# Kernel optimization log

Measured on AMD Instinct MI355X. Metric: run time of the kernel, lower is better.

Reference implementation:

```python
import jax, jax.numpy as jnp
import numpy as np

NEG_INF = -1e30
EPS = 1e-7  # keras.backend.epsilon()

B, T, C, L = 256, 1024, 128, 128


def setup_inputs() -> dict:
    key = jax.random.key(0)
    k1, k2, k3, k4 = jax.random.split(key, 4)
    # ctc_batch_cost expects softmax probabilities in y_pred
    y_pred = jax.nn.softmax(jax.random.normal(k1, (B, T, C), dtype=jnp.float32), axis=-1)
    y_true = jax.random.randint(k2, (B, L), 0, C - 1)           # blank = C-1 excluded from labels
    input_length = jax.random.randint(k3, (B, 1), T // 2, T + 1)
    label_length = jax.random.randint(k4, (B, 1), L // 2, L + 1)
    return {"y_true": y_true, "y_pred": y_pred,
            "input_length": input_length, "label_length": label_length}


def _ctc_batch_cost(y_true, y_pred, input_length, label_length):
    """Faithful jax version of keras.backend.ctc_batch_cost (blank = num_classes-1)."""
    b, t_max, c = y_pred.shape
    l_max = y_true.shape[1]
    s_max = 2 * l_max + 1
    blank = c - 1

    logp = jnp.log(y_pred + EPS)                                # [B,T,C]

    # Extended label sequence: blank, l0, blank, l1, ..., blank  -> [B,S]
    ext = jnp.full((b, s_max), blank, dtype=y_true.dtype)
    ext = ext.at[:, 1::2].set(y_true)

    # Gather log-probs of extended labels per time step -> [B,T,S]
    lp_ext = jnp.take_along_axis(logp, ext[:, None, :], axis=2)

    # Skip transition (s-2 -> s) allowed iff ext[s] != blank and ext[s] != ext[s-2]
    same = jnp.concatenate([jnp.ones((b, 2), bool), ext[:, 2:] == ext[:, :-2]], axis=1)
    skip_ok = (ext != blank) & (~same)                          # [B,S]

    # Valid extended positions given per-sample label_length
    s_idx = jnp.arange(s_max)
    valid_s = s_idx[None, :] < (2 * label_length + 1)           # [B,S]

    ll = label_length[:, 0]
    il = input_length[:, 0]

    alpha0 = jnp.full((b, s_max), NEG_INF, dtype=logp.dtype)
    alpha0 = alpha0.at[:, 0].set(lp_ext[:, 0, 0])
    alpha0 = alpha0.at[:, 1].set(jnp.where(ll > 0, lp_ext[:, 0, 1], NEG_INF))

    neg1 = jnp.full((b, 1), NEG_INF, dtype=logp.dtype)
    neg2 = jnp.full((b, 2), NEG_INF, dtype=logp.dtype)

    def step(alpha, inputs):
        lp_t, t = inputs                                        # lp_t: [B,S]
        a1 = alpha
        a2 = jnp.concatenate([neg1, alpha[:, :-1]], axis=1)
        a3 = jnp.where(skip_ok, jnp.concatenate([neg2, alpha[:, :-2]], axis=1), NEG_INF)
        m = jnp.maximum(jnp.maximum(a1, a2), a3)
        new = m + jnp.log(jnp.exp(a1 - m) + jnp.exp(a2 - m) + jnp.exp(a3 - m)) + lp_t
        new = jnp.where(valid_s, new, NEG_INF)
        alpha = jnp.where((t < il)[:, None], new, alpha)        # freeze past input_length
        return alpha, None

    lp_seq = jnp.moveaxis(lp_ext, 1, 0)[1:]                     # [T-1,B,S]
    ts = jnp.arange(1, t_max)
    alpha_T, _ = jax.lax.scan(step, alpha0, (lp_seq, ts))

    end = 2 * ll                                                # index of final blank
    a_end = jnp.take_along_axis(alpha_T, end[:, None], axis=1)[:, 0]
    a_pen = jnp.take_along_axis(alpha_T, jnp.maximum(end - 1, 0)[:, None], axis=1)[:, 0]
    a_pen = jnp.where(ll > 0, a_pen, NEG_INF)
    loglik = jnp.logaddexp(a_end, a_pen)
    return -loglik[:, None]                                     # [B,1], as ctc_batch_cost


def reference(y_true, y_pred, input_length, label_length):
    # CTCLayer.call computes the loss (add_loss) and returns y_pred; for the
    # kernel baseline we return the loss itself, which is the actual compute.
    return _ctc_batch_cost(y_true, y_pred, input_length, label_length)
```

## Files before the change

kernel.cpp:

```cpp
#include <hip/hip_runtime.h>


constexpr int   Tn    = 1024;
constexpr int   Cc    = 128;
constexpr int   Ln    = 128;
constexpr float EPSf  = 1e-7f;
constexpr int   CK    = 8;
constexpr int   NSLOT = 4;

__device__ __forceinline__ int dpp_max_i32(int m) {
    int o;
    o = __builtin_amdgcn_update_dpp(0, m, 0x111, 0xf, 0xf, false); m = o > m ? o : m;
    o = __builtin_amdgcn_update_dpp(0, m, 0x112, 0xf, 0xf, false); m = o > m ? o : m;
    o = __builtin_amdgcn_update_dpp(0, m, 0x114, 0xf, 0xf, false); m = o > m ? o : m;
    o = __builtin_amdgcn_update_dpp(0, m, 0x118, 0xf, 0xf, false); m = o > m ? o : m;
    o = __builtin_amdgcn_update_dpp(0, m, 0x142, 0xf, 0xf, false); m = o > m ? o : m;
    o = __builtin_amdgcn_update_dpp(0, m, 0x143, 0xf, 0xf, false); m = o > m ? o : m;
    return m;
}

__device__ __forceinline__ double dpp_shr1_f64(double x) {
    const int lo = __double2loint(x), hi = __double2hiint(x);
    const int slo = __builtin_amdgcn_update_dpp(0, lo, 0x138, 0xf, 0xf, true);
    const int shi = __builtin_amdgcn_update_dpp(0, hi, 0x138, 0xf, 0xf, true);
    return __hiloint2double(shi, slo);
}

__global__ __launch_bounds__(128, 1)
void ctc_fwd_kernel(const int*   __restrict__ y_true,
                    const float* __restrict__ y_pred,
                    const int*   __restrict__ in_len,
                    const int*   __restrict__ lab_len,
                    float*       __restrict__ out)
{
    const int tid = threadIdx.x;
    const int L   = tid & 63;
    const int b   = blockIdx.x;
    const int il  = in_len[b];
    const int ll  = lab_len[b];
    const int blank = Cc - 1;

    const int* yb   = y_true + (size_t)b * Ln;
    const int  lab1 = yb[2 * L];
    const int  lab2 = yb[2 * L + 1];

    const float* base = y_pred + (size_t)b * Tn * Cc;
    const int steps = (il > 0) ? (il - 1) : 0;
    const int nfull = steps / CK;
    const int nch   = (steps + CK - 1) / CK;

    __shared__ float  ldsL1[NSLOT][CK][64];
    __shared__ float  ldsL2[NSLOT][CK][64];
    __shared__ float  ldsBK[NSLOT][CK];
    __shared__ double sA[258];

#define BARRIER() do {                                                  \
    __builtin_amdgcn_sched_barrier(0);                                  \
    asm volatile("" ::: "memory");                                      \
    __builtin_amdgcn_s_barrier();                                       \
    asm volatile("" ::: "memory");                                      \
    __builtin_amdgcn_sched_barrier(0);                                  \
} while (0)

#define WAIT_VM(n) do {                                                 \
    __builtin_amdgcn_sched_barrier(0);                                  \
    asm volatile("s_waitcnt vmcnt(" #n ")");                            \
    __builtin_amdgcn_sched_barrier(0);                                  \
} while (0)

    if (tid >= 64) {
#define ISSUE_CHUNK(k) do {                                             \
    const int slot_ = (k) & (NSLOT - 1);                                \
    {                                                                   \
        int tb_ = 1 + (k) * CK + L; if (tb_ > steps) tb_ = steps; if (tb_ < 0) tb_ = 0; \
        const float* g_ = base + (size_t)tb_ * Cc + blank;              \
        if (L < CK)                                                     \
            __builtin_amdgcn_global_load_lds(                           \
                (const __attribute__((address_space(1))) void*)g_,      \
                (__attribute__((address_space(3))) void*)&ldsBK[slot_][0], 4, 0, 0); \
    }                                                                   \
    _Pragma("unroll")                                                   \
    for (int r_ = 0; r_ < CK; ++r_) {                                   \
        int t_ = 1 + (k) * CK + r_; if (t_ > steps) t_ = steps; if (t_ < 0) t_ = 0; \
        const float* row_ = base + (size_t)t_ * Cc;                     \
        __builtin_amdgcn_global_load_lds(                               \
            (const __attribute__((address_space(1))) void*)(row_ + lab1), \
            (__attribute__((address_space(3))) void*)&ldsL1[slot_][r_][0], 4, 0, 0); \
        __builtin_amdgcn_global_load_lds(                               \
            (const __attribute__((address_space(1))) void*)(row_ + lab2), \
            (__attribute__((address_space(3))) void*)&ldsL2[slot_][r_][0], 4, 0, 0); \
    }                                                                   \
} while (0)

        ISSUE_CHUNK(0);
        ISSUE_CHUNK(1);
        WAIT_VM(17);
        BARRIER();
        for (int i = 0; i < nch; ++i) {
            if (i + 2 < nch) {
                ISSUE_CHUNK(i + 2);
                WAIT_VM(17);
            } else {
                WAIT_VM(0);
            }
            BARRIER();
        }
        return;
#undef ISSUE_CHUNK
    }

    const int  labp = (L > 0) ? yb[2 * L - 1] : -1;
    const double skm1 = ((L > 0) && (lab1 != blank) && (lab1 != labp)) ? 1.0 : 0.0;
    const double skm3 = ((lab2 != blank) && (lab2 != lab1)) ? 1.0 : 0.0;

    double a0 = 0.0, a1v = 0.0, a2v = 0.0, a3v = 0.0, a4v = 0.0;
    if (L == 0) {
        a0  = (double)(base[blank] + EPSf);
        a1v = (ll > 0) ? (double)(base[lab1] + EPSf) : 0.0;
    }
    int shift = 0;

#define DPSTEP(gb_, g1_, g2_) do {                                      \
    const double pa3_ = dpp_shr1_f64(a3v);                              \
    const double qb_ = (double)((gb_) + EPSf);                          \
    const double q1_ = (double)((g1_) + EPSf);                          \
    const double q2_ = (double)((g2_) + EPSf);                          \
    const double n0_ = (a0 + pa3_) * qb_;                               \
    const double n1_ = fma(skm1, pa3_, a0 + a1v) * q1_;                 \
    const double n2_ = (a2v + a1v) * qb_;                               \
    const double n3_ = fma(skm3, a1v, a3v + a2v) * q2_;                 \
    const double n4_ = (a4v + a3v) * qb_;                               \
    a0 = n0_; a1v = n1_; a2v = n2_; a3v = n3_; a4v = n4_;               \
} while (0)

#define RESCALE() do {                                                  \
    double m_ = fmax(fmax(a0, a1v), fmax(a2v, a3v)); m_ = fmax(m_, a4v);\
    int be_ = (__double2hiint(m_) >> 20) & 0x7ff;                       \
    be_ = dpp_max_i32(be_);                                             \
    const int emax_ = __builtin_amdgcn_readlane(be_, 63);               \
    const double sc_ = __hiloint2double((2046 - emax_) << 20, 0);       \
    a0 *= sc_; a1v *= sc_; a2v *= sc_; a3v *= sc_; a4v *= sc_;          \
    shift += emax_ - 1023;                                              \
} while (0)

    BARRIER();

    for (int i = 0; i < nch; ++i) {
        const int slot = i & (NSLOT - 1);
        if (i < nfull) {
#pragma unroll
            for (int r = 0; r < CK; ++r)
                DPSTEP(ldsBK[slot][r], ldsL1[slot][r][L], ldsL2[slot][r][L]);
        } else {
#pragma unroll
            for (int r = 0; r < CK; ++r) {
                if (1 + i * CK + r <= steps)
                    DPSTEP(ldsBK[slot][r], ldsL1[slot][r][L], ldsL2[slot][r][L]);
            }
        }
        RESCALE();
        BARRIER();
    }

    sA[4 * L + 0] = a0;
    sA[4 * L + 1] = a1v;
    sA[4 * L + 2] = a2v;
    sA[4 * L + 3] = a3v;
    if (L == 63) sA[256] = a4v;

    if (L == 0) {
        const int end = 2 * ll;
        const double ae = sA[end];
        int pi = end - 1; if (pi < 0) pi = 0;
        double ap = sA[pi];
        if (ll <= 0) ap = 0.0;
        const double s  = ae + ap;
        const double lg = log2(s) + (double)shift;
        out[b] = (float)(-0.6931471805599453 * lg);
    }

#undef BARRIER
#undef WAIT_VM
#undef DPSTEP
#undef RESCALE
}

extern "C" void kernel_launch(void* const* d_in, const int* in_sizes, int n_in,
                              void* d_out, int out_size, void* d_ws, size_t ws_size,
                              hipStream_t stream) {
    const int*   y_true  = (const int*)  d_in[0];
    const float* y_pred  = (const float*)d_in[1];
    const int*   in_len  = (const int*)  d_in[2];
    const int*   lab_len = (const int*)  d_in[3];
    float*       out     = (float*)      d_out;

    ctc_fwd_kernel<<<dim3(256), dim3(128), 0, stream>>>(y_true, y_pred, in_len, lab_len, out);
}
```

Before: 64.26 us.

## Offload eps-add and f64 conversion to producer wave, deepen prefetch, rescale less often

The producer wave now converts each staged chunk of float probabilities (plus epsilon) to double in separate LDS buffers one chunk ahead, so the compute wave's serial DP loop only does FMAs on preconverted values. The prefetch depth grows from two to three chunks in flight, and the per-chunk exponent rescale now runs every other chunk (and on the last one). This costs more LDS and 64-bit LDS reads in the critical loop. Rescaling half as often accepts more dynamic range growth in double between rescales.

```diff
diff --git a/kernel.cpp b/kernel.cpp
--- a/kernel.cpp
+++ b/kernel.cpp
@@ -49,9 +49,12 @@
     const int nfull = steps / CK;
     const int nch   = (steps + CK - 1) / CK;
 
-    __shared__ float  ldsL1[NSLOT][CK][64];
-    __shared__ float  ldsL2[NSLOT][CK][64];
-    __shared__ float  ldsBK[NSLOT][CK];
+    __shared__ float  f32L1[NSLOT][CK][64];
+    __shared__ float  f32L2[NSLOT][CK][64];
+    __shared__ float  f32BK[NSLOT][CK];
+    __shared__ double q64L1[NSLOT][CK][64];
+    __shared__ double q64L2[NSLOT][CK][64];
+    __shared__ double q64BK[NSLOT][CK];
     __shared__ double sA[258];
 
 #define BARRIER() do {                                                  \
@@ -65,6 +68,12 @@
 #define WAIT_VM(n) do {                                                 \
     __builtin_amdgcn_sched_barrier(0);                                  \
     asm volatile("s_waitcnt vmcnt(" #n ")");                            \
+    __builtin_amdgcn_sched_barrier(0);                                  \
+} while (0)
+
+#define WAIT_LGKM0() do {                                               \
+    __builtin_amdgcn_sched_barrier(0);                                  \
+    asm volatile("s_waitcnt lgkmcnt(0)");                               \
     __builtin_amdgcn_sched_barrier(0);                                  \
 } while (0)
 
@@ -77,7 +86,7 @@
         if (L < CK)                                                     \
             __builtin_amdgcn_global_load_lds(                           \
                 (const __attribute__((address_space(1))) void*)g_,      \
-                (__attribute__((address_space(3))) void*)&ldsBK[slot_][0], 4, 0, 0); \
+                (__attribute__((address_space(3))) void*)&f32BK[slot_][0], 4, 0, 0); \
     }                                                                   \
     _Pragma("unroll")                                                   \
     for (int r_ = 0; r_ < CK; ++r_) {                                   \
@@ -85,28 +94,44 @@
         const float* row_ = base + (size_t)t_ * Cc;                     \
         __builtin_amdgcn_global_load_lds(                               \
             (const __attribute__((address_space(1))) void*)(row_ + lab1), \
-            (__attribute__((address_space(3))) void*)&ldsL1[slot_][r_][0], 4, 0, 0); \
+            (__attribute__((address_space(3))) void*)&f32L1[slot_][r_][0], 4, 0, 0); \
         __builtin_amdgcn_global_load_lds(                               \
             (const __attribute__((address_space(1))) void*)(row_ + lab2), \
-            (__attribute__((address_space(3))) void*)&ldsL2[slot_][r_][0], 4, 0, 0); \
+            (__attribute__((address_space(3))) void*)&f32L2[slot_][r_][0], 4, 0, 0); \
     }                                                                   \
+} while (0)
+
+#define CONVERT(k) do {                                                 \
+    const int slot_ = (k) & (NSLOT - 1);                                \
+    _Pragma("unroll")                                                   \
+    for (int r_ = 0; r_ < CK; ++r_) {                                   \
+        q64L1[slot_][r_][L] = (double)(f32L1[slot_][r_][L] + EPSf);     \
+        q64L2[slot_][r_][L] = (double)(f32L2[slot_][r_][L] + EPSf);     \
+    }                                                                   \
+    if (L < CK) q64BK[slot_][L] = (double)(f32BK[slot_][L] + EPSf);     \
 } while (0)
 
         ISSUE_CHUNK(0);
         ISSUE_CHUNK(1);
-        WAIT_VM(17);
+        ISSUE_CHUNK(2);
+        WAIT_VM(34);
+        CONVERT(0);
+        WAIT_LGKM0();
         BARRIER();
         for (int i = 0; i < nch; ++i) {
-            if (i + 2 < nch) {
-                ISSUE_CHUNK(i + 2);
-                WAIT_VM(17);
+            if (i + 3 < nch) {
+                ISSUE_CHUNK(i + 3);
+                WAIT_VM(34);
             } else {
                 WAIT_VM(0);
             }
+            if (i + 1 < nch) CONVERT(i + 1);
+            WAIT_LGKM0();
             BARRIER();
         }
         return;
 #undef ISSUE_CHUNK
+#undef CONVERT
     }
 
     const int  labp = (L > 0) ? yb[2 * L - 1] : -1;
@@ -120,16 +145,13 @@
     }
     int shift = 0;
 
-#define DPSTEP(gb_, g1_, g2_) do {                                      \
+#define DPSTEP(qb_, q1_, q2_) do {                                      \
     const double pa3_ = dpp_shr1_f64(a3v);                              \
-    const double qb_ = (double)((gb_) + EPSf);                          \
-    const double q1_ = (double)((g1_) + EPSf);                          \
-    const double q2_ = (double)((g2_) + EPSf);                          \
-    const double n0_ = (a0 + pa3_) * qb_;                               \
-    const double n1_ = fma(skm1, pa3_, a0 + a1v) * q1_;                 \
-    const double n2_ = (a2v + a1v) * qb_;                               \
-    const double n3_ = fma(skm3, a1v, a3v + a2v) * q2_;                 \
-    const double n4_ = (a4v + a3v) * qb_;                               \
+    const double n0_ = (a0 + pa3_) * (qb_);                             \
+    const double n1_ = fma(skm1, pa3_, a0 + a1v) * (q1_);               \
+    const double n2_ = (a2v + a1v) * (qb_);                             \
+    const double n3_ = fma(skm3, a1v, a3v + a2v) * (q2_);               \
+    const double n4_ = (a4v + a3v) * (qb_);                             \
     a0 = n0_; a1v = n1_; a2v = n2_; a3v = n3_; a4v = n4_;               \
 } while (0)
 
@@ -150,15 +172,15 @@
         if (i < nfull) {
 #pragma unroll
             for (int r = 0; r < CK; ++r)
-                DPSTEP(ldsBK[slot][r], ldsL1[slot][r][L], ldsL2[slot][r][L]);
+                DPSTEP(q64BK[slot][r], q64L1[slot][r][L], q64L2[slot][r][L]);
         } else {
 #pragma unroll
             for (int r = 0; r < CK; ++r) {
                 if (1 + i * CK + r <= steps)
-                    DPSTEP(ldsBK[slot][r], ldsL1[slot][r][L], ldsL2[slot][r][L]);
+                    DPSTEP(q64BK[slot][r], q64L1[slot][r][L], q64L2[slot][r][L]);
             }
         }
-        RESCALE();
+        if ((i & 1) || (i == nch - 1)) RESCALE();
         BARRIER();
     }
 
@@ -181,6 +203,7 @@
 
 #undef BARRIER
 #undef WAIT_VM
+#undef WAIT_LGKM0
 #undef DPSTEP
 #undef RESCALE
 }
```

Result: slower. 106.0 us (+65.0%).
